# Kernel optimization log

Hardware: AMD Instinct MI355X
Metric: run time of the kernel (lower is better)

## Reference

```python
import jax, jax.numpy as jnp
import numpy as np

B, N, C, H, W = 64, 500, 256, 64, 64


def grid_sample_bilinear(im, pts):
    """torch.grid_sample bilinear, align_corners=True, padding_mode='zeros'.
    im: [B,C,H,W]; pts: [B,N,2] (x,y) in [-1,1] -> [B,C,N]."""
    b, c, h, w = im.shape
    x = (pts[..., 0] + 1.0) * 0.5 * (w - 1)  # [B,N]
    y = (pts[..., 1] + 1.0) * 0.5 * (h - 1)
    x0 = jnp.floor(x); y0 = jnp.floor(y)
    x1 = x0 + 1.0; y1 = y0 + 1.0
    wx1 = x - x0; wx0 = 1.0 - wx1
    wy1 = y - y0; wy0 = 1.0 - wy1
    flat = im.reshape(b, c, h * w)

    def gather(xi, yi):
        inb = (xi >= 0) & (xi <= w - 1) & (yi >= 0) & (yi <= h - 1)
        xc = jnp.clip(xi, 0, w - 1).astype(jnp.int32)
        yc = jnp.clip(yi, 0, h - 1).astype(jnp.int32)
        idx = (yc * w + xc)[:, None, :]  # [B,1,N]
        g = jnp.take_along_axis(flat, idx, axis=2)  # [B,C,N]
        return g * inb[:, None, :].astype(im.dtype)

    return (gather(x0, y0) * (wx0 * wy0)[:, None, :]
            + gather(x1, y0) * (wx1 * wy0)[:, None, :]
            + gather(x0, y1) * (wx0 * wy1)[:, None, :]
            + gather(x1, y1) * (wx1 * wy1)[:, None, :])


def setup_inputs() -> dict:
    key = jax.random.key(0)
    ks = jax.random.split(key, 12)
    p = jax.random.uniform(ks[0], (B, N, 2), jnp.float32, -1.0, 1.0)
    s_feat = jax.random.normal(ks[1], (B, C, H, W), jnp.float32)
    def conv_p(k, co, ci):
        k1, k2 = jax.random.split(k)
        s = 1.0 / np.sqrt(ci)
        return (jax.random.uniform(k1, (co, ci), jnp.float32, -s, s),
                jax.random.uniform(k2, (co,), jnp.float32, -s, s))
    w0, b0 = conv_p(ks[2], 128, 256)
    w1, b1 = conv_p(ks[3], 64, 128 + 256)
    w2, b2 = conv_p(ks[4], 5, 64 + 256)
    fc_w, fc_b = conv_p(ks[5], 236, 5 * N)
    return {"p": p, "s_feat": s_feat, "w0": w0, "b0": b0, "w1": w1, "b1": b1,
            "w2": w2, "b2": b2, "fc_w": fc_w, "fc_b": fc_b}


def reference(p, s_feat, w0, b0, w1, b1, w2, b2, fc_w, fc_b):
    feat = grid_sample_bilinear(s_feat, p)  # [B,256,N]
    y = jnp.einsum('oc,bcn->bon', w0, feat) + b0[None, :, None]
    y = jax.nn.leaky_relu(y, 0.01)
    y = jnp.einsum('oc,bcn->bon', w1, jnp.concatenate([y, feat], axis=1)) + b1[None, :, None]
    y = jax.nn.leaky_relu(y, 0.01)
    y = jnp.einsum('oc,bcn->bon', w2, jnp.concatenate([y, feat], axis=1)) + b2[None, :, None]
    y = jax.nn.relu(y)           # last_op
    y = y.reshape(y.shape[0], -1)  # [B, 5*N]
    return y @ fc_w.T + fc_b       # [B, 236]
```

## Files before the change

### kernel.cpp

```cpp
#include <hip/hip_runtime.h>
#include <hip/hip_bf16.h>

#define BB 64
#define NN 500
#define CC 256
#define HH 64
#define WW 64
#define HWSZ 4096
#define NPTS 32000
#define NPAD 512

typedef __attribute__((ext_vector_type(4))) short s4v;
typedef __attribute__((ext_vector_type(8))) short s8v;
typedef __attribute__((ext_vector_type(4))) float f4v;
typedef __attribute__((ext_vector_type(4))) int i4v;

__device__ __forceinline__ unsigned short bfround(float f) {
    unsigned u = __builtin_bit_cast(unsigned, f);
    return (unsigned short)((u + 0x7FFFu + ((u >> 16) & 1u)) >> 16);
}

#define GATHER_BLKS 1024
#define NCHB 16
#define W0F_N 32768
#define W1F_N 24576
#define W2F_N 5120
#define PACK_N (W0F_N + W1F_N + W2F_N)
#define FCT_N 590000
#define PACKALL_N (PACK_N + FCT_N)
#define PACK_BLKS ((PACKALL_N + 511) / 512)

__global__ __launch_bounds__(512) void k_gp(const float* __restrict__ sfeat,
                                            const float* __restrict__ pts,
                                            const float* __restrict__ w0,
                                            const float* __restrict__ w1,
                                            const float* __restrict__ w2,
                                            const float* __restrict__ fcw,
                                            unsigned int* __restrict__ featB,
                                            unsigned short* __restrict__ w0f,
                                            unsigned short* __restrict__ w1f,
                                            unsigned short* __restrict__ w2f,
                                            float* __restrict__ fcwT) {
    __shared__ float im[2][HWSZ];
    const int blk = blockIdx.x;
    const int tid = threadIdx.x;

    if (blk >= GATHER_BLKS) {
        int i = (blk - GATHER_BLKS) * 512 + tid;
        if (i < W0F_N) {
            int j = i & 7, ll = (i >> 3) & 63, s = (i >> 9) & 7, m = i >> 12;
            int row = m * 16 + (ll & 15), k = s * 32 + (ll >> 4) * 8 + j;
            w0f[i] = bfround(w0[row * 256 + k]);
        } else if (i < W0F_N + W1F_N) {
            int d = i - W0F_N;
            int j = d & 7, ll = (d >> 3) & 63, rest = d >> 9;
            int s = rest % 12, m = rest / 12;
            int row = m * 16 + (ll & 15), k = s * 32 + (ll >> 4) * 8 + j;
            w1f[d] = bfround(w1[row * 384 + k]);
        } else if (i < PACK_N) {
            int d = i - (W0F_N + W1F_N);
            int j = d & 7, ll = (d >> 3) & 63, s = d >> 9;
            int row = ll & 15, k = s * 32 + (ll >> 4) * 8 + j;
            float v = (row < 5) ? w2[row * 320 + k] : 0.f;
            w2f[d] = bfround(v);
        } else if (i < PACKALL_N) {
            int d = i - PACK_N;
            int k = d / 236, o = d - k * 236;
            fcwT[d] = fcw[o * 2500 + k];
        }
        return;
    }

    const int b     = blk >> 4;
    const int chunk = blk & 15;
    const int ch0   = chunk * NCHB;
    const int n     = tid;

    int4 id = make_int4(0, 0, 0, 0);
    float4 wt = make_float4(0.f, 0.f, 0.f, 0.f);
    if (n < NN) {
        float x = (pts[((size_t)b * NN + n) * 2 + 0] + 1.f) * 0.5f * (float)(WW - 1);
        float y = (pts[((size_t)b * NN + n) * 2 + 1] + 1.f) * 0.5f * (float)(HH - 1);
        float x0f = floorf(x), y0f = floorf(y);
        float x1f = x0f + 1.f, y1f = y0f + 1.f;
        float wx1 = x - x0f, wx0 = 1.f - wx1;
        float wy1 = y - y0f, wy0 = 1.f - wy1;
        float mx0 = (x0f >= 0.f && x0f <= (float)(WW - 1)) ? 1.f : 0.f;
        float mx1 = (x1f >= 0.f && x1f <= (float)(WW - 1)) ? 1.f : 0.f;
        float my0 = (y0f >= 0.f && y0f <= (float)(HH - 1)) ? 1.f : 0.f;
        float my1 = (y1f >= 0.f && y1f <= (float)(HH - 1)) ? 1.f : 0.f;
        int x0 = (int)fminf(fmaxf(x0f, 0.f), (float)(WW - 1));
        int x1 = (int)fminf(fmaxf(x1f, 0.f), (float)(WW - 1));
        int y0 = (int)fminf(fmaxf(y0f, 0.f), (float)(HH - 1));
        int y1 = (int)fminf(fmaxf(y1f, 0.f), (float)(HH - 1));
        id = make_int4(y0 * WW + x0, y0 * WW + x1, y1 * WW + x0, y1 * WW + x1);
        wt = make_float4(wx0 * wy0 * mx0 * my0, wx1 * wy0 * mx1 * my0,
                         wx0 * wy1 * mx0 * my1, wx1 * wy1 * mx1 * my1);
    }

    const float4* src = (const float4*)(sfeat + ((size_t)b * CC + ch0) * HWSZ);

#pragma unroll
    for (int it = 0; it < 2; it++) {
        int j = it * 512 + tid;
        __builtin_amdgcn_global_load_lds(
            (const __attribute__((address_space(1))) void*)(src + j),
            (__attribute__((address_space(3))) void*)((float4*)im[0] + j),
            16, 0, 0);
    }

    unsigned short hprev = 0;
    for (int t = 0; t < NCHB; t++) {
        if (t + 1 < NCHB) {
            const float4* s2 = src + (size_t)(t + 1) * (HWSZ / 4);
            float4* dst = (float4*)im[(t + 1) & 1];
#pragma unroll
            for (int it = 0; it < 2; it++) {
                int j = it * 512 + tid;
                __builtin_amdgcn_global_load_lds(
                    (const __attribute__((address_space(1))) void*)(s2 + j),
                    (__attribute__((address_space(3))) void*)(dst + j),
                    16, 0, 0);
            }
            asm volatile("s_waitcnt vmcnt(2)" ::: "memory");
        } else {
            asm volatile("s_waitcnt vmcnt(0)" ::: "memory");
        }
        asm volatile("s_barrier" ::: "memory");

        if (n < NN) {
            const float* L = im[t & 1];
            float r = wt.x * L[id.x] + wt.y * L[id.y] + wt.z * L[id.z] + wt.w * L[id.w];
            unsigned short h = bfround(r);
            if (t & 1) {
                unsigned int v = (unsigned int)hprev | ((unsigned int)h << 16);
                int kg = chunk * 2 + (t >> 3);
                int jp = (t & 7) >> 1;
                featB[(((size_t)b * 32 + kg) * 4 + jp) * 512 + n] = v;
            } else {
                hprev = h;
            }
        }
        if (t + 1 < NCHB)
            asm volatile("s_barrier" ::: "memory");
    }
}

#define K1_S 136
#define K2_S 72

__device__ __forceinline__ s8v mkfrag(const unsigned short* p) {
    return *(const s8v*)p;
}

__global__ __launch_bounds__(512, 4) void k_mlp(const unsigned int* __restrict__ featB,
                                                const unsigned short* __restrict__ w0f,
                                                const unsigned short* __restrict__ w1f,
                                                const unsigned short* __restrict__ w2f,
                                                const float* __restrict__ b0,
                                                const float* __restrict__ b1,
                                                const float* __restrict__ b2,
                                                float* __restrict__ y2f) {
    __shared__ unsigned short c1B[32 * K1_S];
    __shared__ unsigned short c2B[32 * K2_S];

    const int b   = blockIdx.y;
    const int n0  = blockIdx.x * 32;
    const int tid = threadIdx.x;
    const int w   = tid >> 6, l = tid & 63;
    const int nt  = w & 1, mh = w >> 1;
    const int lo16 = l & 15, hi = l >> 4;
    const int c = nt * 16 + lo16;

    s8v bhs[8];
    const unsigned int* fb = featB + (size_t)b * (32 * 4 * 512) + (n0 + c);
#pragma unroll
    for (int s = 0; s < 8; s++) {
        const int kg = s * 4 + hi;
        i4v hx;
#pragma unroll
        for (int t = 0; t < 4; t++)
            hx[t] = (int)fb[(size_t)(kg * 4 + t) * 512];
        bhs[s] = __builtin_bit_cast(s8v, hx);
    }

    f4v acc0 = {0.f, 0.f, 0.f, 0.f}, acc1 = {0.f, 0.f, 0.f, 0.f};
#pragma unroll
    for (int s = 0; s < 8; s++) {
        const s8v a0 = mkfrag(w0f + ((size_t)((mh * 2) * 8 + s) * 64 + l) * 8);
        const s8v a1 = mkfrag(w0f + ((size_t)((mh * 2 + 1) * 8 + s) * 64 + l) * 8);
        acc0 = __builtin_amdgcn_mfma_f32_16x16x32_bf16(a0, bhs[s], acc0, 0, 0, 0);
        acc1 = __builtin_amdgcn_mfma_f32_16x16x32_bf16(a1, bhs[s], acc1, 0, 0, 0);
    }
#pragma unroll
    for (int m = 0; m < 2; m++) {
#pragma unroll
        for (int r = 0; r < 4; r++) {
            int ch = (mh * 2 + m) * 16 + hi * 4 + r;
            float v = (m ? acc1[r] : acc0[r]) + b0[ch];
            v = v > 0.f ? v : 0.01f * v;
            c1B[c * K1_S + ch] = bfround(v);
        }
    }
    __syncthreads();

    f4v accA = {0.f, 0.f, 0.f, 0.f};
#pragma unroll
    for (int s = 0; s < 4; s++) {
        const s8v bh = *(const s8v*)&c1B[c * K1_S + s * 32 + hi * 8];
        const s8v a  = mkfrag(w1f + ((size_t)(mh * 12 + s) * 64 + l) * 8);
        accA = __builtin_amdgcn_mfma_f32_16x16x32_bf16(a, bh, accA, 0, 0, 0);
    }
#pragma unroll
    for (int s = 4; s < 12; s++) {
        const s8v a = mkfrag(w1f + ((size_t)(mh * 12 + s) * 64 + l) * 8);
        accA = __builtin_amdgcn_mfma_f32_16x16x32_bf16(a, bhs[s - 4], accA, 0, 0, 0);
    }
#pragma unroll
    for (int r = 0; r < 4; r++) {
        int ch = mh * 16 + hi * 4 + r;
        float v = accA[r] + b1[ch];
        v = v > 0.f ? v : 0.01f * v;
        c2B[c * K2_S + ch] = bfround(v);
    }
    __syncthreads();

    if (mh == 0) {
        f4v acc2 = {0.f, 0.f, 0.f, 0.f};
#pragma unroll
        for (int s = 0; s < 2; s++) {
            const s8v bh = *(const s8v*)&c2B[c * K2_S + s * 32 + hi * 8];
            const s8v a  = mkfrag(w2f + ((size_t)s * 64 + l) * 8);
            acc2 = __builtin_amdgcn_mfma_f32_16x16x32_bf16(a, bh, acc2, 0, 0, 0);
        }
#pragma unroll
        for (int s = 2; s < 10; s++) {
            const s8v a = mkfrag(w2f + ((size_t)s * 64 + l) * 8);
            acc2 = __builtin_amdgcn_mfma_f32_16x16x32_bf16(a, bhs[s - 2], acc2, 0, 0, 0);
        }
#pragma unroll
        for (int r = 0; r < 4; r++) {
            int ch = hi * 4 + r;
            if (ch < 5) {
                float v = acc2[r] + b2[ch];
                v = fmaxf(v, 0.f);
                int n = n0 + c;
                if (n < NN) y2f[(size_t)b * 2500 + ch * NN + n] = v;
            }
        }
    }
}

__global__ __launch_bounds__(256) void k_fc1(const float* __restrict__ y2f,
                                             const float* __restrict__ fcwT,
                                             float* __restrict__ part) {
    __shared__ float ys[313];
    const int b  = blockIdx.x & 63;
    const int kc = blockIdx.x >> 6;
    const int start = kc * 312 + (kc < 4 ? kc : 4);
    const int len   = (kc < 4) ? 313 : 312;
    const float* yb = y2f + (size_t)b * 2500 + start;
    for (int j = threadIdx.x; j < len; j += 256) ys[j] = yb[j];
    __syncthreads();
    const int o = threadIdx.x;
    if (o < 236) {
        float acc = 0.f;
        const float* wp = fcwT + (size_t)start * 236 + o;
#pragma unroll 8
        for (int k = 0; k < len; k++) acc = fmaf(wp[(size_t)k * 236], ys[k], acc);
        part[((size_t)kc * 64 + b) * 236 + o] = acc;
    }
}

__global__ __launch_bounds__(256) void k_fc2(const float* __restrict__ part,
                                             const float* __restrict__ fcb,
                                             float* __restrict__ out) {
    const int b = blockIdx.x;
    const int o = threadIdx.x;
    if (o < 236) {
        float acc = fcb[o];
#pragma unroll
        for (int kc = 0; kc < 8; kc++) acc += part[((size_t)kc * 64 + b) * 236 + o];
        out[b * 236 + o] = acc;
    }
}

extern "C" void kernel_launch(void* const* d_in, const int* in_sizes, int n_in,
                              void* d_out, int out_size, void* d_ws, size_t ws_size,
                              hipStream_t stream) {
    const float* p   = (const float*)d_in[0];
    const float* sf  = (const float*)d_in[1];
    const float* w0  = (const float*)d_in[2];
    const float* b0  = (const float*)d_in[3];
    const float* w1  = (const float*)d_in[4];
    const float* b1  = (const float*)d_in[5];
    const float* w2  = (const float*)d_in[6];
    const float* b2  = (const float*)d_in[7];
    const float* fcw = (const float*)d_in[8];
    const float* fcb = (const float*)d_in[9];
    float* out = (float*)d_out;

    char* ws = (char*)d_ws;
    unsigned int*   featB = (unsigned int*)(ws);
    float*          y2f   = (float*)(ws + 16777216);
    float*          fcwT  = (float*)(ws + 17417216);
    float*          part  = (float*)(ws + 19777216);
    unsigned short* w0f   = (unsigned short*)(ws + 20260544);
    unsigned short* w1f   = (unsigned short*)(ws + 20326080);
    unsigned short* w2f   = (unsigned short*)(ws + 20375232);

    k_gp<<<GATHER_BLKS + PACK_BLKS, 512, 0, stream>>>(sf, p, w0, w1, w2, fcw,
                                                      featB, w0f, w1f, w2f, fcwT);
    k_mlp<<<dim3(16, BB), 512, 0, stream>>>(featB, w0f, w1f, w2f,
                                            b0, b1, b2, y2f);
    k_fc1<<<512, 256, 0, stream>>>(y2f, fcwT, part);
    k_fc2<<<BB, 256, 0, stream>>>(part, fcb, out);
}
```

Measured before the change: 82.89 us.

## Triple-buffer gather prefetch, halve channels per block, fuse FC into one kernel

The gather kernel now uses 8 channels per block with twice as many blocks and a three-buffer LDS ring that keeps two channel loads in flight, aiming to hide more global latency and expose more parallelism. The fcw transpose pass is dropped from the pack blocks. The two-stage FC (k_fc1 partial sums plus k_fc2 reduce) becomes a single kernel that reads fcw rows directly and reduces each output with a wave shuffle. This removes one launch and the transpose traffic. In exchange the gather uses more LDS per block (48KB), which may lower occupancy, and the FC rereads fcw for each batch without the transposed coalescing.

```diff
diff --git a/kernel.cpp b/kernel.cpp
--- a/kernel.cpp
+++ b/kernel.cpp
@@ -20,28 +20,25 @@
     return (unsigned short)((u + 0x7FFFu + ((u >> 16) & 1u)) >> 16);
 }
 
-#define GATHER_BLKS 1024
-#define NCHB 16
+#define GATHER_BLKS 2048
+#define NCHB 8
+#define NBUF 3
 #define W0F_N 32768
 #define W1F_N 24576
 #define W2F_N 5120
 #define PACK_N (W0F_N + W1F_N + W2F_N)
-#define FCT_N 590000
-#define PACKALL_N (PACK_N + FCT_N)
-#define PACK_BLKS ((PACKALL_N + 511) / 512)
+#define PACK_BLKS ((PACK_N + 511) / 512)
 
 __global__ __launch_bounds__(512) void k_gp(const float* __restrict__ sfeat,
                                             const float* __restrict__ pts,
                                             const float* __restrict__ w0,
                                             const float* __restrict__ w1,
                                             const float* __restrict__ w2,
-                                            const float* __restrict__ fcw,
                                             unsigned int* __restrict__ featB,
                                             unsigned short* __restrict__ w0f,
                                             unsigned short* __restrict__ w1f,
-                                            unsigned short* __restrict__ w2f,
-                                            float* __restrict__ fcwT) {
-    __shared__ float im[2][HWSZ];
+                                            unsigned short* __restrict__ w2f) {
+    __shared__ float im[NBUF][HWSZ];
     const int blk = blockIdx.x;
     const int tid = threadIdx.x;
 
@@ -63,16 +60,12 @@
             int row = ll & 15, k = s * 32 + (ll >> 4) * 8 + j;
             float v = (row < 5) ? w2[row * 320 + k] : 0.f;
             w2f[d] = bfround(v);
-        } else if (i < PACKALL_N) {
-            int d = i - PACK_N;
-            int k = d / 236, o = d - k * 236;
-            fcwT[d] = fcw[o * 2500 + k];
         }
         return;
     }
 
-    const int b     = blk >> 4;
-    const int chunk = blk & 15;
+    const int b     = blk >> 5;
+    const int chunk = blk & 31;
     const int ch0   = chunk * NCHB;
     const int n     = tid;
 
@@ -100,28 +93,29 @@
 
     const float4* src = (const float4*)(sfeat + ((size_t)b * CC + ch0) * HWSZ);
 
-#pragma unroll
-    for (int it = 0; it < 2; it++) {
-        int j = it * 512 + tid;
-        __builtin_amdgcn_global_load_lds(
-            (const __attribute__((address_space(1))) void*)(src + j),
-            (__attribute__((address_space(3))) void*)((float4*)im[0] + j),
-            16, 0, 0);
-    }
+#define ISSUE_CH(T, BUF)                                                      \
+    {                                                                         \
+        const float4* s2 = src + (size_t)(T) * (HWSZ / 4);                    \
+        float4* dst = (float4*)im[BUF];                                       \
+        _Pragma("unroll")                                                     \
+        for (int it = 0; it < 2; it++) {                                      \
+            int j = it * 512 + tid;                                           \
+            __builtin_amdgcn_global_load_lds(                                 \
+                (const __attribute__((address_space(1))) void*)(s2 + j),      \
+                (__attribute__((address_space(3))) void*)(dst + j),           \
+                16, 0, 0);                                                    \
+        }                                                                     \
+    }
+
+    ISSUE_CH(0, 0);
+    ISSUE_CH(1, 1);
 
     unsigned short hprev = 0;
     for (int t = 0; t < NCHB; t++) {
-        if (t + 1 < NCHB) {
-            const float4* s2 = src + (size_t)(t + 1) * (HWSZ / 4);
-            float4* dst = (float4*)im[(t + 1) & 1];
-#pragma unroll
-            for (int it = 0; it < 2; it++) {
-                int j = it * 512 + tid;
-                __builtin_amdgcn_global_load_lds(
-                    (const __attribute__((address_space(1))) void*)(s2 + j),
-                    (__attribute__((address_space(3))) void*)(dst + j),
-                    16, 0, 0);
-            }
+        if (t + 2 < NCHB) {
+            ISSUE_CH(t + 2, (t + 2) % 3);
+            asm volatile("s_waitcnt vmcnt(4)" ::: "memory");
+        } else if (t + 1 < NCHB) {
             asm volatile("s_waitcnt vmcnt(2)" ::: "memory");
         } else {
             asm volatile("s_waitcnt vmcnt(0)" ::: "memory");
@@ -129,14 +123,12 @@
         asm volatile("s_barrier" ::: "memory");
 
         if (n < NN) {
-            const float* L = im[t & 1];
+            const float* L = im[t % 3];
             float r = wt.x * L[id.x] + wt.y * L[id.y] + wt.z * L[id.z] + wt.w * L[id.w];
             unsigned short h = bfround(r);
             if (t & 1) {
                 unsigned int v = (unsigned int)hprev | ((unsigned int)h << 16);
-                int kg = chunk * 2 + (t >> 3);
-                int jp = (t & 7) >> 1;
-                featB[(((size_t)b * 32 + kg) * 4 + jp) * 512 + n] = v;
+                featB[(((size_t)b * 32 + chunk) * 4 + (t >> 1)) * 512 + n] = v;
             } else {
                 hprev = h;
             }
@@ -144,6 +136,7 @@
         if (t + 1 < NCHB)
             asm volatile("s_barrier" ::: "memory");
     }
+#undef ISSUE_CH
 }
 
 #define K1_S 136
@@ -251,37 +244,26 @@
     }
 }
 
-__global__ __launch_bounds__(256) void k_fc1(const float* __restrict__ y2f,
-                                             const float* __restrict__ fcwT,
-                                             float* __restrict__ part) {
-    __shared__ float ys[313];
+__global__ __launch_bounds__(256) void k_fc(const float* __restrict__ y2f,
+                                            const float* __restrict__ fcw,
+                                            const float* __restrict__ fcb,
+                                            float* __restrict__ out) {
+    __shared__ float ys[2500];
     const int b  = blockIdx.x & 63;
-    const int kc = blockIdx.x >> 6;
-    const int start = kc * 312 + (kc < 4 ? kc : 4);
-    const int len   = (kc < 4) ? 313 : 312;
-    const float* yb = y2f + (size_t)b * 2500 + start;
-    for (int j = threadIdx.x; j < len; j += 256) ys[j] = yb[j];
+    const int oc = blockIdx.x >> 6;
+    for (int j = threadIdx.x; j < 2500; j += 256) ys[j] = y2f[(size_t)b * 2500 + j];
     __syncthreads();
-    const int o = threadIdx.x;
-    if (o < 236) {
+
+    const int wv = threadIdx.x >> 6;
+    const int lane = threadIdx.x & 63;
+    for (int oi = wv; oi < 59; oi += 4) {
+        int o = oc * 59 + oi;
         float acc = 0.f;
-        const float* wp = fcwT + (size_t)start * 236 + o;
-#pragma unroll 8
-        for (int k = 0; k < len; k++) acc = fmaf(wp[(size_t)k * 236], ys[k], acc);
-        part[((size_t)kc * 64 + b) * 236 + o] = acc;
-    }
-}
-
-__global__ __launch_bounds__(256) void k_fc2(const float* __restrict__ part,
-                                             const float* __restrict__ fcb,
-                                             float* __restrict__ out) {
-    const int b = blockIdx.x;
-    const int o = threadIdx.x;
-    if (o < 236) {
-        float acc = fcb[o];
-#pragma unroll
-        for (int kc = 0; kc < 8; kc++) acc += part[((size_t)kc * 64 + b) * 236 + o];
-        out[b * 236 + o] = acc;
+        const float* wp = fcw + (size_t)o * 2500;
+        for (int j = lane; j < 2500; j += 64) acc = fmaf(wp[j], ys[j], acc);
+#pragma unroll
+        for (int off = 32; off > 0; off >>= 1) acc += __shfl_down(acc, off);
+        if (lane == 0) out[b * 236 + o] = acc + fcb[o];
     }
 }
 
@@ -303,16 +285,13 @@
     char* ws = (char*)d_ws;
     unsigned int*   featB = (unsigned int*)(ws);
     float*          y2f   = (float*)(ws + 16777216);
-    float*          fcwT  = (float*)(ws + 17417216);
-    float*          part  = (float*)(ws + 19777216);
-    unsigned short* w0f   = (unsigned short*)(ws + 20260544);
-    unsigned short* w1f   = (unsigned short*)(ws + 20326080);
-    unsigned short* w2f   = (unsigned short*)(ws + 20375232);
-
-    k_gp<<<GATHER_BLKS + PACK_BLKS, 512, 0, stream>>>(sf, p, w0, w1, w2, fcw,
-                                                      featB, w0f, w1f, w2f, fcwT);
+    unsigned short* w0f   = (unsigned short*)(ws + 17417216);
+    unsigned short* w1f   = (unsigned short*)(ws + 17482752);
+    unsigned short* w2f   = (unsigned short*)(ws + 17531904);
+
+    k_gp<<<GATHER_BLKS + PACK_BLKS, 512, 0, stream>>>(sf, p, w0, w1, w2,
+                                                      featB, w0f, w1f, w2f);
     k_mlp<<<dim3(16, BB), 512, 0, stream>>>(featB, w0f, w1f, w2f,
                                             b0, b1, b2, y2f);
-    k_fc1<<<512, 256, 0, stream>>>(y2f, fcwT, part);
-    k_fc2<<<BB, 256, 0, stream>>>(part, fcb, out);
-}
+    k_fc<<<256, 256, 0, stream>>>(y2f, fcw, fcb, out);
+}
```

New measurement: 232.5 us. +180.5%, slower.
